# Optimization experiments

Hardware: AMD Instinct MI355X
Metric: run time of the kernel (lower is better)

## Reference

```python
import jax, jax.numpy as jnp
import numpy as np

B, S, HID, NH, HD = 2, 2048, 768, 12, 64
WINDOW = 128           # ModernBERT local attention window
ROPE_THETA = 10000.0   # local_rope_theta (layer_index=0 -> is_local_attention=True)


def _rotate_half(x):
    x1, x2 = jnp.split(x, 2, axis=-1)
    return jnp.concatenate([-x2, x1], axis=-1)


def setup_inputs() -> dict:
    key = jax.random.key(0)
    k1, k2, k3 = jax.random.split(key, 3)
    hidden_embed = jax.random.normal(k1, (B, S, HID), dtype=jnp.float32)
    Wq = jax.random.normal(k2, (HID, HID), dtype=jnp.float32) * (HID ** -0.5)
    Wo = jax.random.normal(k3, (HID, HID), dtype=jnp.float32) * (HID ** -0.5)
    position_index = jnp.arange(S, dtype=jnp.int32).reshape(1, S)
    # sliding-window additive mask: 0 inside window, -inf outside
    i = jnp.arange(S)
    dist = jnp.abs(i[:, None] - i[None, :])
    local_attention_mask = jnp.where(dist <= WINDOW // 2, 0.0, -jnp.inf).astype(jnp.float32)[None, None]
    global_attention_mask = jnp.zeros((1, 1, S, S), dtype=jnp.float32)
    return {
        "hidden_embed": hidden_embed,
        "Wq": Wq,
        "Wo": Wo,
        "local_attention_mask": local_attention_mask,
        "global_attention_mask": global_attention_mask,
        "position_index": position_index,
    }


def reference(hidden_embed, Wq, Wo, local_attention_mask, global_attention_mask, position_index):
    # q projection; NOTE: source has k = q.view(...), v = q.view(...) -> k and v ARE q
    q = hidden_embed @ Wq.T                                  # [B,S,HID]
    q = q.reshape(B, S, NH, HD).transpose(0, 2, 1, 3)        # [B,NH,S,HD]

    # RoPE
    inv_freq = 1.0 / (ROPE_THETA ** (jnp.arange(0, HD, 2, dtype=jnp.float32) / HD))  # [HD/2]
    pos = position_index.reshape(-1).astype(jnp.float32)     # [S]
    freqs = pos[:, None] * inv_freq[None, :]                 # [S,HD/2]
    emb = jnp.concatenate([freqs, freqs], axis=-1)           # [S,HD]
    cos, sin = jnp.cos(emb), jnp.sin(emb)
    q_rot = q * cos + _rotate_half(q) * sin                  # [B,NH,S,HD]
    k_rot = q_rot                                            # k == q before rope -> same after rope
    v = q                                                    # v == q (no rope on v)

    # masked SDPA (local layer -> local sliding-window mask)
    scale = jnp.asarray(HD, jnp.float32) ** -0.5
    scores = jnp.einsum('bhtd,bhsd->bhts', q_rot, k_rot) * scale + local_attention_mask
    attn = jax.nn.softmax(scores, axis=-1)                   # [B,NH,S,S]
    out = jnp.einsum('bhts,bhsd->bhtd', attn, v)             # [B,NH,S,HD]
    out = out.transpose(0, 2, 1, 3).reshape(B, S, HID)
    return out @ Wo.T
```

## Files before the change

kernel.cpp:

```cpp
#include <hip/hip_runtime.h>
#include <hip/hip_bf16.h>
#include <math.h>
#include <stdint.h>

#define B_    2
#define S_    2048
#define HID_  768
#define NH_   12
#define HD_   64
#define NROWS (B_ * S_)
#define N_HID_ELEM (NROWS * HID_)
#define N_W_ELEM   (HID_ * HID_)

#define KW   224
#define KSTR 232

typedef __bf16 bf16x8 __attribute__((ext_vector_type(8)));
typedef float  floatx4 __attribute__((ext_vector_type(4)));

__global__ void convert_inputs_kernel(const float* __restrict__ src_hidden,
                                      const float* __restrict__ src_w1,
                                      const float* __restrict__ src_w2,
                                      __hip_bfloat16* __restrict__ Hb,
                                      __hip_bfloat16* __restrict__ Wqb,
                                      __hip_bfloat16* __restrict__ Wob)
{
    int i = blockIdx.x * blockDim.x + threadIdx.x;
    const float* src;
    __hip_bfloat16* dst;
    int off;
    const int NH4 = N_HID_ELEM / 4, NW4 = N_W_ELEM / 4;
    if (i < NH4)           { src = src_hidden; dst = Hb;  off = i; }
    else if (i < NH4+NW4)  { src = src_w1;     dst = Wqb; off = i - NH4; }
    else if (i < NH4+2*NW4){ src = src_w2;     dst = Wob; off = i - NH4 - NW4; }
    else return;
    float4 v = reinterpret_cast<const float4*>(src)[off];
    __hip_bfloat16 o[4] = { __float2bfloat16(v.x), __float2bfloat16(v.y),
                            __float2bfloat16(v.z), __float2bfloat16(v.w) };
    *reinterpret_cast<uint64_t*>(dst + 4 * (size_t)off) = *reinterpret_cast<uint64_t*>(o);
}

__device__ __forceinline__ void gload_lds16(const __hip_bfloat16* g, __hip_bfloat16* l)
{
    __builtin_amdgcn_global_load_lds(
        (const __attribute__((address_space(1))) void*)g,
        (__attribute__((address_space(3))) void*)l, 16, 0, 0);
}

template<int MODE>
__global__ __launch_bounds__(256) void gemm64(
    const __hip_bfloat16* __restrict__ A,
    const __hip_bfloat16* __restrict__ W,
    __hip_bfloat16* __restrict__ C,
    __hip_bfloat16* __restrict__ C2,
    float* __restrict__ Cf,
    const int* __restrict__ pos_idx,
    int M, int N, int K)
{
    __shared__ __align__(16) __hip_bfloat16 Alds[2][64][32];
    __shared__ __align__(16) __hip_bfloat16 Wlds[2][64][32];

    const int tid  = threadIdx.x;
    const int wv   = tid >> 6;
    const int lane = tid & 63;
    const int l16  = lane & 15;
    const int quad = lane >> 4;
    const int m0 = blockIdx.x * 64;
    const int n0 = blockIdx.y * 64;

    const int c   = wv * 64 + lane;
    const int sr  = c >> 2;
    const int sc8 = (c & 3) * 8;

    const __hip_bfloat16* gA0 = A + (size_t)(m0 + sr) * K + sc8;
    const __hip_bfloat16* gA1 = A + (size_t)(m0 + sr) * K + 32 + sc8;
    const __hip_bfloat16* gW0 = W + (size_t)(n0 + sr) * K + sc8;
    const __hip_bfloat16* gW1 = W + (size_t)(n0 + sr) * K + 32 + sc8;
    __hip_bfloat16* lA0 = &Alds[0][wv * 16][0];
    __hip_bfloat16* lA1 = &Alds[1][wv * 16][0];
    __hip_bfloat16* lW0 = &Wlds[0][wv * 16][0];
    __hip_bfloat16* lW1 = &Wlds[1][wv * 16][0];

    floatx4 acc[4] = {};
    const int ra = wv * 16 + l16;

    for (int k0 = 0; k0 < K; k0 += 64) {
        gload_lds16(gA0 + k0, lA0);
        gload_lds16(gA1 + k0, lA1);
        gload_lds16(gW0 + k0, lW0);
        gload_lds16(gW1 + k0, lW1);
        __syncthreads();

#pragma unroll
        for (int ks = 0; ks < 2; ++ks) {
            bf16x8 a = *reinterpret_cast<const bf16x8*>(&Alds[ks][ra][quad * 8]);
#pragma unroll
            for (int u = 0; u < 4; ++u) {
                bf16x8 w = *reinterpret_cast<const bf16x8*>(&Wlds[ks][u * 16 + l16][quad * 8]);
                acc[u] = __builtin_amdgcn_mfma_f32_16x16x32_bf16(a, w, acc[u], 0, 0, 0);
            }
        }
        __syncthreads();
    }

    if (MODE == 1) {
#pragma unroll
        for (int r = 0; r < 4; ++r) {
            int m = m0 + wv * 16 + quad * 4 + r;
            int s = m & (S_ - 1);
            float pos = (float)pos_idx[s];
#pragma unroll
            for (int u = 0; u < 2; ++u) {
                float f = (float)(u * 16 + l16);
                float inv = exp2f(f * (-0.41524101186092024f));
                float sn, cs;
                sincosf(pos * inv, &sn, &cs);
                float q0 = acc[u][r];
                float q1 = acc[u + 2][r];
                size_t base = (size_t)m * HID_ + n0 + u * 16 + l16;
                C [base]      = __float2bfloat16(q0);
                C [base + 32] = __float2bfloat16(q1);
                C2[base]      = __float2bfloat16(q0 * cs - q1 * sn);
                C2[base + 32] = __float2bfloat16(q1 * cs + q0 * sn);
            }
        }
    } else {
#pragma unroll
        for (int u = 0; u < 4; ++u)
#pragma unroll
            for (int r = 0; r < 4; ++r) {
                int row = m0 + wv * 16 + quad * 4 + r;
                int col = n0 + u * 16 + l16;
                Cf[(size_t)row * N + col] = acc[u][r];
            }
    }
}

__global__ __launch_bounds__(256) void attn_kernel(
    const __hip_bfloat16* __restrict__ Q,
    const __hip_bfloat16* __restrict__ Qr,
    __hip_bfloat16* __restrict__ O)
{
    __shared__ __align__(16) __hip_bfloat16 Vt[64][KSTR];
    __shared__ __align__(16) __hip_bfloat16 Pl[64][KSTR];

    const int bh = blockIdx.y;
    const int b  = bh / NH_;
    const int h  = bh % NH_;
    const int i0 = blockIdx.x * 64;
    const int tid = threadIdx.x;

    for (int idx = tid; idx < KW * 64; idx += 256) {
        int w = idx >> 6;
        int d = idx & 63;
        int j = i0 - 64 + w;
        int jc = min(max(j, 0), S_ - 1);
        Vt[d][w] = Q[((size_t)(b * S_ + jc)) * HID_ + h * HD_ + d];
    }
    __syncthreads();

    const int wv   = tid >> 6;
    const int lane = tid & 63;
    const int l16  = lane & 15;
    const int quad = lane >> 4;

    floatx4 sc[10] = {};
    const __hip_bfloat16* qrow =
        Qr + ((size_t)(b * S_ + i0 + wv * 16 + l16)) * HID_ + h * HD_ + quad * 8;
#pragma unroll
    for (int ks = 0; ks < 2; ++ks) {
        bf16x8 a = *reinterpret_cast<const bf16x8*>(qrow + ks * 32);
#pragma unroll
        for (int t = 0; t < 10; ++t) {
            int j = i0 - 64 + (wv + t) * 16 + l16;
            int jc = min(max(j, 0), S_ - 1);
            bf16x8 bfr = *reinterpret_cast<const bf16x8*>(
                Qr + ((size_t)(b * S_ + jc)) * HID_ + h * HD_ + ks * 32 + quad * 8);
            sc[t] = __builtin_amdgcn_mfma_f32_16x16x32_bf16(a, bfr, sc[t], 0, 0, 0);
        }
    }

    const float scale = 0.125f;
    float denom[4];
#pragma unroll
    for (int r = 0; r < 4; ++r) {
        const int R = wv * 16 + quad * 4 + r;
        float xv[10];
        float mx = -3.0e38f;
#pragma unroll
        for (int t = 0; t < 10; ++t) {
            int w = (wv + t) * 16 + l16;
            int j = i0 - 64 + w;
            bool valid = (w >= R) && (w <= R + 128) && (j >= 0) && (j < S_);
            float x = valid ? sc[t][r] * scale : -1.0e30f;
            xv[t] = x;
            mx = fmaxf(mx, x);
        }
#pragma unroll
        for (int msk = 1; msk < 16; msk <<= 1) mx = fmaxf(mx, __shfl_xor(mx, msk, 64));
        float sum = 0.f;
#pragma unroll
        for (int t = 0; t < 10; ++t) {
            float p = __expf(xv[t] - mx);
            sum += p;
            Pl[R][(wv + t) * 16 + l16] = __float2bfloat16(p);
        }
#pragma unroll
        for (int msk = 1; msk < 16; msk <<= 1) sum += __shfl_xor(sum, msk, 64);
        denom[r] = sum;
    }
    __syncthreads();

    floatx4 oacc[4] = {};
#pragma unroll
    for (int c = 0; c < 5; ++c) {
        const int base = wv * 16 + c * 32;
        bf16x8 a = *reinterpret_cast<const bf16x8*>(&Pl[wv * 16 + l16][base + quad * 8]);
#pragma unroll
        for (int u = 0; u < 4; ++u) {
            bf16x8 bfr = *reinterpret_cast<const bf16x8*>(&Vt[u * 16 + l16][base + quad * 8]);
            oacc[u] = __builtin_amdgcn_mfma_f32_16x16x32_bf16(a, bfr, oacc[u], 0, 0, 0);
        }
    }

#pragma unroll
    for (int u = 0; u < 4; ++u)
#pragma unroll
        for (int r = 0; r < 4; ++r) {
            int row = i0 + wv * 16 + quad * 4 + r;
            int col = u * 16 + l16;
            O[((size_t)(b * S_ + row)) * HID_ + h * HD_ + col] =
                __float2bfloat16(oacc[u][r] / denom[r]);
        }
}

extern "C" void kernel_launch(void* const* d_in, const int* in_sizes, int n_in,
                              void* d_out, int out_size, void* d_ws, size_t ws_size,
                              hipStream_t stream)
{
    int ih = -1, iw1 = -1, iw2 = -1, ip = -1;
    for (int i = 0; i < n_in; ++i) {
        int s = in_sizes[i];
        if      (s == N_HID_ELEM && ih < 0) ih = i;
        else if (s == N_W_ELEM)  { if (iw1 < 0) iw1 = i; else if (iw2 < 0) iw2 = i; }
        else if (s == S_ && ip < 0) ip = i;
    }
    if (ih < 0)  ih = 0;
    if (iw1 < 0) iw1 = 1;
    if (iw2 < 0) iw2 = 2;
    if (ip < 0)  ip = 5;

    const float* hidden = (const float*)d_in[ih];
    const float* w1     = (const float*)d_in[iw1];
    const float* w2     = (const float*)d_in[iw2];
    const int*   pos    = (const int*)d_in[ip];

    __hip_bfloat16* Hb  = (__hip_bfloat16*)d_ws;
    __hip_bfloat16* Wqb = Hb  + N_HID_ELEM;
    __hip_bfloat16* Wob = Wqb + N_W_ELEM;
    __hip_bfloat16* Q   = Wob + N_W_ELEM;
    __hip_bfloat16* Qr  = Q   + N_HID_ELEM;
    __hip_bfloat16* AO  = Hb;

    int conv4 = (N_HID_ELEM + 2 * N_W_ELEM) / 4;
    convert_inputs_kernel<<<(conv4 + 255) / 256, 256, 0, stream>>>(
        hidden, w1, w2, Hb, Wqb, Wob);

    dim3 gblk(NROWS / 64, HID_ / 64);

    gemm64<1><<<gblk, 256, 0, stream>>>(Hb, Wqb, Q, Qr, nullptr, pos,
                                        NROWS, HID_, HID_);

    attn_kernel<<<dim3(S_ / 64, B_ * NH_), 256, 0, stream>>>(Q, Qr, AO);

    gemm64<2><<<gblk, 256, 0, stream>>>(AO, Wob, nullptr, nullptr, (float*)d_out,
                                        nullptr, NROWS, HID_, HID_);
}
```

Measured before the change: 145.9 us.

## Fuse fp32-to-bf16 input conversion into GEMM tile loads

Removes the separate conversion kernel. Each GEMM now reads fp32 activations and weights directly from global memory, converts them in registers, and stores bf16 into a padded LDS tile with row stride 72. This saves one kernel launch and a round trip through the bf16 workspace. In exchange, the async global-to-LDS loads become synchronous register loads, and each weight tile is read as fp32 by every block, roughly doubling weight traffic per tile.

```diff
diff --git a/kernel.cpp b/kernel.cpp
--- a/kernel.cpp
+++ b/kernel.cpp
@@ -14,51 +14,51 @@
 
 #define KW   224
 #define KSTR 232
+#define LSTR 72
 
 typedef __bf16 bf16x8 __attribute__((ext_vector_type(8)));
 typedef float  floatx4 __attribute__((ext_vector_type(4)));
 
-__global__ void convert_inputs_kernel(const float* __restrict__ src_hidden,
-                                      const float* __restrict__ src_w1,
-                                      const float* __restrict__ src_w2,
-                                      __hip_bfloat16* __restrict__ Hb,
-                                      __hip_bfloat16* __restrict__ Wqb,
-                                      __hip_bfloat16* __restrict__ Wob)
-{
-    int i = blockIdx.x * blockDim.x + threadIdx.x;
-    const float* src;
-    __hip_bfloat16* dst;
-    int off;
-    const int NH4 = N_HID_ELEM / 4, NW4 = N_W_ELEM / 4;
-    if (i < NH4)           { src = src_hidden; dst = Hb;  off = i; }
-    else if (i < NH4+NW4)  { src = src_w1;     dst = Wqb; off = i - NH4; }
-    else if (i < NH4+2*NW4){ src = src_w2;     dst = Wob; off = i - NH4 - NW4; }
-    else return;
-    float4 v = reinterpret_cast<const float4*>(src)[off];
-    __hip_bfloat16 o[4] = { __float2bfloat16(v.x), __float2bfloat16(v.y),
-                            __float2bfloat16(v.z), __float2bfloat16(v.w) };
-    *reinterpret_cast<uint64_t*>(dst + 4 * (size_t)off) = *reinterpret_cast<uint64_t*>(o);
-}
-
-__device__ __forceinline__ void gload_lds16(const __hip_bfloat16* g, __hip_bfloat16* l)
-{
-    __builtin_amdgcn_global_load_lds(
-        (const __attribute__((address_space(1))) void*)g,
-        (__attribute__((address_space(3))) void*)l, 16, 0, 0);
-}
-
-template<int MODE>
+__device__ __forceinline__ void cvt_store16(const float* __restrict__ g,
+                                            __hip_bfloat16* __restrict__ l)
+{
+    floatx4 v0 = *reinterpret_cast<const floatx4*>(g);
+    floatx4 v1 = *reinterpret_cast<const floatx4*>(g + 4);
+    floatx4 v2 = *reinterpret_cast<const floatx4*>(g + 8);
+    floatx4 v3 = *reinterpret_cast<const floatx4*>(g + 12);
+    __hip_bfloat16 o[16];
+#pragma unroll
+    for (int i = 0; i < 4; ++i) {
+        o[i]      = __float2bfloat16(v0[i]);
+        o[4 + i]  = __float2bfloat16(v1[i]);
+        o[8 + i]  = __float2bfloat16(v2[i]);
+        o[12 + i] = __float2bfloat16(v3[i]);
+    }
+    *reinterpret_cast<bf16x8*>(l)     = *reinterpret_cast<bf16x8*>(o);
+    *reinterpret_cast<bf16x8*>(l + 8) = *reinterpret_cast<bf16x8*>(o + 8);
+}
+
+__device__ __forceinline__ void copy_store16(const __hip_bfloat16* __restrict__ g,
+                                             __hip_bfloat16* __restrict__ l)
+{
+    bf16x8 v0 = *reinterpret_cast<const bf16x8*>(g);
+    bf16x8 v1 = *reinterpret_cast<const bf16x8*>(g + 8);
+    *reinterpret_cast<bf16x8*>(l)     = v0;
+    *reinterpret_cast<bf16x8*>(l + 8) = v1;
+}
+
+template<int ROPE>
 __global__ __launch_bounds__(256) void gemm64(
-    const __hip_bfloat16* __restrict__ A,
-    const __hip_bfloat16* __restrict__ W,
+    const void* __restrict__ Araw,
+    const float* __restrict__ Wf,
     __hip_bfloat16* __restrict__ C,
     __hip_bfloat16* __restrict__ C2,
     float* __restrict__ Cf,
     const int* __restrict__ pos_idx,
     int M, int N, int K)
 {
-    __shared__ __align__(16) __hip_bfloat16 Alds[2][64][32];
-    __shared__ __align__(16) __hip_bfloat16 Wlds[2][64][32];
+    __shared__ __align__(16) __hip_bfloat16 Alds[64 * LSTR];
+    __shared__ __align__(16) __hip_bfloat16 Wlds[64 * LSTR];
 
     const int tid  = threadIdx.x;
     const int wv   = tid >> 6;
@@ -68,42 +68,40 @@
     const int m0 = blockIdx.x * 64;
     const int n0 = blockIdx.y * 64;
 
-    const int c   = wv * 64 + lane;
-    const int sr  = c >> 2;
-    const int sc8 = (c & 3) * 8;
-
-    const __hip_bfloat16* gA0 = A + (size_t)(m0 + sr) * K + sc8;
-    const __hip_bfloat16* gA1 = A + (size_t)(m0 + sr) * K + 32 + sc8;
-    const __hip_bfloat16* gW0 = W + (size_t)(n0 + sr) * K + sc8;
-    const __hip_bfloat16* gW1 = W + (size_t)(n0 + sr) * K + 32 + sc8;
-    __hip_bfloat16* lA0 = &Alds[0][wv * 16][0];
-    __hip_bfloat16* lA1 = &Alds[1][wv * 16][0];
-    __hip_bfloat16* lW0 = &Wlds[0][wv * 16][0];
-    __hip_bfloat16* lW1 = &Wlds[1][wv * 16][0];
+    const int trow = tid >> 2;
+    const int tk   = (tid & 3) * 16;
+
+    const float* gW            = Wf + (size_t)(n0 + trow) * K + tk;
+    const float* gAf           = (const float*)Araw + (size_t)(m0 + trow) * K + tk;
+    const __hip_bfloat16* gAb  = (const __hip_bfloat16*)Araw + (size_t)(m0 + trow) * K + tk;
+
+    __hip_bfloat16* lA = &Alds[trow * LSTR + tk];
+    __hip_bfloat16* lW = &Wlds[trow * LSTR + tk];
 
     floatx4 acc[4] = {};
     const int ra = wv * 16 + l16;
 
     for (int k0 = 0; k0 < K; k0 += 64) {
-        gload_lds16(gA0 + k0, lA0);
-        gload_lds16(gA1 + k0, lA1);
-        gload_lds16(gW0 + k0, lW0);
-        gload_lds16(gW1 + k0, lW1);
+        if (ROPE) cvt_store16(gAf + k0, lA);
+        else      copy_store16(gAb + k0, lA);
+        cvt_store16(gW + k0, lW);
         __syncthreads();
 
 #pragma unroll
         for (int ks = 0; ks < 2; ++ks) {
-            bf16x8 a = *reinterpret_cast<const bf16x8*>(&Alds[ks][ra][quad * 8]);
+            bf16x8 a = *reinterpret_cast<const bf16x8*>(
+                &Alds[ra * LSTR + ks * 32 + quad * 8]);
 #pragma unroll
             for (int u = 0; u < 4; ++u) {
-                bf16x8 w = *reinterpret_cast<const bf16x8*>(&Wlds[ks][u * 16 + l16][quad * 8]);
+                bf16x8 w = *reinterpret_cast<const bf16x8*>(
+                    &Wlds[(u * 16 + l16) * LSTR + ks * 32 + quad * 8]);
                 acc[u] = __builtin_amdgcn_mfma_f32_16x16x32_bf16(a, w, acc[u], 0, 0, 0);
             }
         }
         __syncthreads();
     }
 
-    if (MODE == 1) {
+    if (ROPE) {
 #pragma unroll
         for (int r = 0; r < 4; ++r) {
             int m = m0 + wv * 16 + quad * 4 + r;
@@ -255,24 +253,17 @@
     const float* w2     = (const float*)d_in[iw2];
     const int*   pos    = (const int*)d_in[ip];
 
-    __hip_bfloat16* Hb  = (__hip_bfloat16*)d_ws;
-    __hip_bfloat16* Wqb = Hb  + N_HID_ELEM;
-    __hip_bfloat16* Wob = Wqb + N_W_ELEM;
-    __hip_bfloat16* Q   = Wob + N_W_ELEM;
-    __hip_bfloat16* Qr  = Q   + N_HID_ELEM;
-    __hip_bfloat16* AO  = Hb;
-
-    int conv4 = (N_HID_ELEM + 2 * N_W_ELEM) / 4;
-    convert_inputs_kernel<<<(conv4 + 255) / 256, 256, 0, stream>>>(
-        hidden, w1, w2, Hb, Wqb, Wob);
+    __hip_bfloat16* Q  = (__hip_bfloat16*)d_ws;
+    __hip_bfloat16* Qr = Q  + N_HID_ELEM;
+    __hip_bfloat16* AO = Qr + N_HID_ELEM;
 
     dim3 gblk(NROWS / 64, HID_ / 64);
 
-    gemm64<1><<<gblk, 256, 0, stream>>>(Hb, Wqb, Q, Qr, nullptr, pos,
+    gemm64<1><<<gblk, 256, 0, stream>>>(hidden, w1, Q, Qr, nullptr, pos,
                                         NROWS, HID_, HID_);
 
     attn_kernel<<<dim3(S_ / 64, B_ * NH_), 256, 0, stream>>>(Q, Qr, AO);
 
-    gemm64<2><<<gblk, 256, 0, stream>>>(AO, Wob, nullptr, nullptr, (float*)d_out,
+    gemm64<0><<<gblk, 256, 0, stream>>>(AO, w2, nullptr, nullptr, (float*)d_out,
                                         nullptr, NROWS, HID_, HID_);
 }
```

After: 160.5 us. 1.1x slower.

## Split-K GEMM with double-buffered LDS and vectorize attention V load/output store

Applied to the files above, without the earlier changes.

The GEMM kernel now runs 512 threads per block, with two K-halves processed by separate 256-thread groups. Each group double-buffers its LDS tiles so the next tile's loads overlap the current MFMAs, and the partial sums are reduced through LDS before the epilogue. In the attention kernel, V is loaded with 16-byte vector reads instead of scalar reads. The output is staged through LDS so it can be written as coalesced 16-byte stores. The aim is more in-flight work and fewer narrow memory transactions, at the cost of extra LDS traffic, an LDS reduction and more barriers.

```diff
diff --git a/kernel.cpp b/kernel.cpp
--- a/kernel.cpp
+++ b/kernel.cpp
@@ -47,8 +47,8 @@
         (__attribute__((address_space(3))) void*)l, 16, 0, 0);
 }
 
-template<int MODE>
-__global__ __launch_bounds__(256) void gemm64(
+template<int ROPE>
+__global__ __launch_bounds__(512) void gemm64k2(
     const __hip_bfloat16* __restrict__ A,
     const __hip_bfloat16* __restrict__ W,
     __hip_bfloat16* __restrict__ C,
@@ -57,56 +57,79 @@
     const int* __restrict__ pos_idx,
     int M, int N, int K)
 {
-    __shared__ __align__(16) __hip_bfloat16 Alds[2][64][32];
-    __shared__ __align__(16) __hip_bfloat16 Wlds[2][64][32];
+    __shared__ __align__(16) __hip_bfloat16 Ald[2][2][2][64][32];
+    __shared__ __align__(16) __hip_bfloat16 Wld[2][2][2][64][32];
 
     const int tid  = threadIdx.x;
-    const int wv   = tid >> 6;
+    const int kg   = tid >> 8;
+    const int wv4  = (tid >> 6) & 3;
     const int lane = tid & 63;
     const int l16  = lane & 15;
     const int quad = lane >> 4;
     const int m0 = blockIdx.x * 64;
     const int n0 = blockIdx.y * 64;
 
-    const int c   = wv * 64 + lane;
+    const int c   = wv4 * 64 + lane;
     const int sr  = c >> 2;
     const int sc8 = (c & 3) * 8;
-
-    const __hip_bfloat16* gA0 = A + (size_t)(m0 + sr) * K + sc8;
-    const __hip_bfloat16* gA1 = A + (size_t)(m0 + sr) * K + 32 + sc8;
-    const __hip_bfloat16* gW0 = W + (size_t)(n0 + sr) * K + sc8;
-    const __hip_bfloat16* gW1 = W + (size_t)(n0 + sr) * K + 32 + sc8;
-    __hip_bfloat16* lA0 = &Alds[0][wv * 16][0];
-    __hip_bfloat16* lA1 = &Alds[1][wv * 16][0];
-    __hip_bfloat16* lW0 = &Wlds[0][wv * 16][0];
-    __hip_bfloat16* lW1 = &Wlds[1][wv * 16][0];
+    const int kbase = kg * 384;
+
+    const __hip_bfloat16* gA = A + (size_t)(m0 + sr) * K + kbase + sc8;
+    const __hip_bfloat16* gW = W + (size_t)(n0 + sr) * K + kbase + sc8;
 
     floatx4 acc[4] = {};
-    const int ra = wv * 16 + l16;
-
-    for (int k0 = 0; k0 < K; k0 += 64) {
-        gload_lds16(gA0 + k0, lA0);
-        gload_lds16(gA1 + k0, lA1);
-        gload_lds16(gW0 + k0, lW0);
-        gload_lds16(gW1 + k0, lW1);
+    const int ra = wv4 * 16 + l16;
+
+    gload_lds16(gA,      &Ald[kg][0][0][wv4 * 16][0]);
+    gload_lds16(gA + 32, &Ald[kg][0][1][wv4 * 16][0]);
+    gload_lds16(gW,      &Wld[kg][0][0][wv4 * 16][0]);
+    gload_lds16(gW + 32, &Wld[kg][0][1][wv4 * 16][0]);
+
+#pragma unroll
+    for (int it = 0; it < 6; ++it) {
+        const int cur = it & 1;
         __syncthreads();
-
+        if (it + 1 < 6) {
+            const int nb = (it + 1) & 1;
+            const int ko = (it + 1) * 64;
+            gload_lds16(gA + ko,      &Ald[kg][nb][0][wv4 * 16][0]);
+            gload_lds16(gA + ko + 32, &Ald[kg][nb][1][wv4 * 16][0]);
+            gload_lds16(gW + ko,      &Wld[kg][nb][0][wv4 * 16][0]);
+            gload_lds16(gW + ko + 32, &Wld[kg][nb][1][wv4 * 16][0]);
+        }
 #pragma unroll
         for (int ks = 0; ks < 2; ++ks) {
-            bf16x8 a = *reinterpret_cast<const bf16x8*>(&Alds[ks][ra][quad * 8]);
+            bf16x8 a = *reinterpret_cast<const bf16x8*>(&Ald[kg][cur][ks][ra][quad * 8]);
 #pragma unroll
             for (int u = 0; u < 4; ++u) {
-                bf16x8 w = *reinterpret_cast<const bf16x8*>(&Wlds[ks][u * 16 + l16][quad * 8]);
+                bf16x8 w = *reinterpret_cast<const bf16x8*>(
+                    &Wld[kg][cur][ks][u * 16 + l16][quad * 8]);
                 acc[u] = __builtin_amdgcn_mfma_f32_16x16x32_bf16(a, w, acc[u], 0, 0, 0);
             }
         }
-        __syncthreads();
-    }
-
-    if (MODE == 1) {
+    }
+
+    __syncthreads();
+    float* Red = reinterpret_cast<float*>(&Ald[0][0][0][0][0]);
+    if (kg == 1) {
+#pragma unroll
+        for (int u = 0; u < 4; ++u)
+#pragma unroll
+            for (int r = 0; r < 4; ++r)
+                Red[(wv4 * 16 + quad * 4 + r) * 68 + u * 16 + l16] = acc[u][r];
+    }
+    __syncthreads();
+    if (kg == 1) return;
+#pragma unroll
+    for (int u = 0; u < 4; ++u)
+#pragma unroll
+        for (int r = 0; r < 4; ++r)
+            acc[u][r] += Red[(wv4 * 16 + quad * 4 + r) * 68 + u * 16 + l16];
+
+    if (ROPE) {
 #pragma unroll
         for (int r = 0; r < 4; ++r) {
-            int m = m0 + wv * 16 + quad * 4 + r;
+            int m = m0 + wv4 * 16 + quad * 4 + r;
             int s = m & (S_ - 1);
             float pos = (float)pos_idx[s];
 #pragma unroll
@@ -129,7 +152,7 @@
         for (int u = 0; u < 4; ++u)
 #pragma unroll
             for (int r = 0; r < 4; ++r) {
-                int row = m0 + wv * 16 + quad * 4 + r;
+                int row = m0 + wv4 * 16 + quad * 4 + r;
                 int col = n0 + u * 16 + l16;
                 Cf[(size_t)row * N + col] = acc[u][r];
             }
@@ -150,12 +173,16 @@
     const int i0 = blockIdx.x * 64;
     const int tid = threadIdx.x;
 
-    for (int idx = tid; idx < KW * 64; idx += 256) {
-        int w = idx >> 6;
-        int d = idx & 63;
-        int j = i0 - 64 + w;
+    for (int idx = tid; idx < KW * 8; idx += 256) {
+        int w  = idx >> 3;
+        int d8 = (idx & 7) * 8;
+        int j  = i0 - 64 + w;
         int jc = min(max(j, 0), S_ - 1);
-        Vt[d][w] = Q[((size_t)(b * S_ + jc)) * HID_ + h * HD_ + d];
+        bf16x8 v = *reinterpret_cast<const bf16x8*>(
+            Q + ((size_t)(b * S_ + jc)) * HID_ + h * HD_ + d8);
+        const __hip_bfloat16* ve = reinterpret_cast<const __hip_bfloat16*>(&v);
+#pragma unroll
+        for (int e = 0; e < 8; ++e) Vt[d8 + e][w] = ve[e];
     }
     __syncthreads();
 
@@ -223,15 +250,25 @@
         }
     }
 
+    __syncthreads();
+    float* Of = reinterpret_cast<float*>(&Pl[0][0]);
 #pragma unroll
     for (int u = 0; u < 4; ++u)
 #pragma unroll
-        for (int r = 0; r < 4; ++r) {
-            int row = i0 + wv * 16 + quad * 4 + r;
-            int col = u * 16 + l16;
-            O[((size_t)(b * S_ + row)) * HID_ + h * HD_ + col] =
-                __float2bfloat16(oacc[u][r] / denom[r]);
-        }
+        for (int r = 0; r < 4; ++r)
+            Of[(wv * 16 + quad * 4 + r) * 68 + u * 16 + l16] = oacc[u][r] / denom[r];
+    __syncthreads();
+    {
+        int row = tid >> 2;
+        int seg = (tid & 3) * 16;
+        __hip_bfloat16 ob[16];
+#pragma unroll
+        for (int e = 0; e < 16; ++e)
+            ob[e] = __float2bfloat16(Of[row * 68 + seg + e]);
+        __hip_bfloat16* dst = O + ((size_t)(b * S_ + i0 + row)) * HID_ + h * HD_ + seg;
+        *reinterpret_cast<bf16x8*>(dst)     = *reinterpret_cast<bf16x8*>(ob);
+        *reinterpret_cast<bf16x8*>(dst + 8) = *reinterpret_cast<bf16x8*>(ob + 8);
+    }
 }
 
 extern "C" void kernel_launch(void* const* d_in, const int* in_sizes, int n_in,
@@ -268,11 +305,11 @@
 
     dim3 gblk(NROWS / 64, HID_ / 64);
 
-    gemm64<1><<<gblk, 256, 0, stream>>>(Hb, Wqb, Q, Qr, nullptr, pos,
-                                        NROWS, HID_, HID_);
+    gemm64k2<1><<<gblk, 512, 0, stream>>>(Hb, Wqb, Q, Qr, nullptr, pos,
+                                          NROWS, HID_, HID_);
 
     attn_kernel<<<dim3(S_ / 64, B_ * NH_), 256, 0, stream>>>(Q, Qr, AO);
 
-    gemm64<2><<<gblk, 256, 0, stream>>>(AO, Wob, nullptr, nullptr, (float*)d_out,
-                                        nullptr, NROWS, HID_, HID_);
-}
+    gemm64k2<0><<<gblk, 512, 0, stream>>>(AO, Wob, nullptr, nullptr, (float*)d_out,
+                                          nullptr, NROWS, HID_, HID_);
+}
```

New measurement: 143.6 us. About the same (-1.6%).
